# Optimization experiments

Hardware: AMD Instinct MI355X
Metric: run time of the kernel (lower is better)

The kernel has to match this reference:

```python
import jax, jax.numpy as jnp
import numpy as np

B, IN, HID, OUT = 16384, 1024, 4096, 1024
E, K, SIG = 8, 2, 32
ROUTER_IN = IN + SIG + 3  # 1059


def setup_inputs() -> dict:
    key = jax.random.key(0)
    ks = jax.random.split(key, 10)
    sc = lambda k, shape, fan_in: (jax.random.normal(k, shape, jnp.float32)
                                   * (1.0 / np.sqrt(fan_in)))
    return {
        "x": jax.random.normal(ks[0], (B, IN), jnp.float32),
        "physical_signature": jax.random.normal(ks[1], (B, SIG), jnp.float32),
        "task_context": jax.random.uniform(ks[2], (B, 1), jnp.float32),
        "resource_state": jax.random.uniform(ks[3], (B, 2), jnp.float32),
        "router_w1": sc(ks[4], (ROUTER_IN, 2 * E), ROUTER_IN),
        "router_b1": jnp.zeros((2 * E,), jnp.float32),
        "router_w2": sc(ks[5], (2 * E, E), 2 * E),
        "router_b2": jnp.zeros((E,), jnp.float32),
        "expert_w1": sc(ks[6], (E, IN, HID), IN),
        "expert_b1": jnp.zeros((E, HID), jnp.float32),
        "expert_w2": sc(ks[7], (E, HID, OUT), HID),
        "expert_b2": jnp.zeros((E, OUT), jnp.float32),
    }


def reference(x, physical_signature, task_context, resource_state,
              router_w1, router_b1, router_w2, router_b2,
              expert_w1, expert_b1, expert_w2, expert_b2):
    # Router: Linear -> GELU(exact) -> Linear over [x; sig; tc; rs]
    combined = jnp.concatenate(
        [x, physical_signature, task_context, resource_state], axis=-1)
    h = jax.nn.gelu(combined @ router_w1 + router_b1, approximate=False)
    logits = h @ router_w2 + router_b2                      # [B, E]
    weights = jax.nn.softmax(logits, axis=-1)
    top_w, top_idx = jax.lax.top_k(weights, K)              # [B, K]
    # Per-token per-expert combine weight (0 if expert not in top-k)
    c = jnp.einsum("bk,bke->be", top_w,
                   jax.nn.one_hot(top_idx, E, dtype=top_w.dtype))  # [B, E]
    # Dispatch/combine: weighted sum of MLP expert outputs (loop over
    # fixed small E; tokens not routed to expert j have c[:, j] == 0)
    out = jnp.zeros((x.shape[0], OUT), x.dtype)
    for j in range(E):
        hj = jax.nn.gelu(x @ expert_w1[j] + expert_b1[j], approximate=False)
        yj = hj @ expert_w2[j] + expert_b2[j]               # [B, OUT]
        out = out + c[:, j:j + 1] * yj
    return out
```

## Files before the change

### kernel.cpp

```cpp
#include <hip/hip_runtime.h>
#include <math.h>


#define B_TOK 16384
#define IN_D 1024
#define HID_D 4096
#define OUT_D 1024
#define NEXP 8
#define SIG_D 32
#define RIN 1059

#define TILE 128
#define BK 16
#define ROWS_MAX 33792

#define CTRL_COUNTS 0
#define CTRL_CURS 8
#define CTRL_OFFS 16

typedef float f32x4 __attribute__((ext_vector_type(4)));
typedef _Float16 f16x8 __attribute__((ext_vector_type(8)));
typedef short s16x8 __attribute__((ext_vector_type(8)));

__device__ __forceinline__ float gelu_exact(float v) {
    return 0.5f * v * (1.0f + erff(v * 0.70710678118654752440f));
}

__device__ __forceinline__ unsigned short f2h(float f) {
    _Float16 h = (_Float16)f;
    unsigned short u;
    __builtin_memcpy(&u, &h, 2);
    return u;
}

__device__ __forceinline__ void gl16(const unsigned short* g, unsigned short* lds) {
    __builtin_amdgcn_global_load_lds(
        (const __attribute__((address_space(1))) void*)g,
        (__attribute__((address_space(3))) void*)lds, 16, 0, 0);
}


__global__ void zero_ctrl_kernel(int* ctrl) {
    if (threadIdx.x < 32) ctrl[threadIdx.x] = 0;
}

__global__ void zero_out_kernel(float4* out, int n4) {
    int i = blockIdx.x * blockDim.x + threadIdx.x;
    int stride = gridDim.x * blockDim.x;
    for (; i < n4; i += stride) out[i] = make_float4(0.f, 0.f, 0.f, 0.f);
}

__global__ __launch_bounds__(256)
void router_kernel(const float* __restrict__ x, const float* __restrict__ sig,
                   const float* __restrict__ tc, const float* __restrict__ rs,
                   const float* __restrict__ rw1, const float* __restrict__ rb1,
                   const float* __restrict__ rw2, const float* __restrict__ rb2,
                   int* __restrict__ ctrl, int* __restrict__ tt_idx,
                   float2* __restrict__ tt_w) {
    const int wave = threadIdx.x >> 6;
    const int lane = threadIdx.x & 63;
    const int t = blockIdx.x * 4 + wave;

    float acc[16];
#pragma unroll
    for (int j = 0; j < 16; ++j) acc[j] = 0.f;

    for (int i = lane; i < RIN; i += 64) {
        float xv;
        if (i < IN_D) xv = x[(size_t)t * IN_D + i];
        else if (i < IN_D + SIG_D) xv = sig[(size_t)t * SIG_D + (i - IN_D)];
        else if (i == IN_D + SIG_D) xv = tc[t];
        else xv = rs[(size_t)t * 2 + (i - (IN_D + SIG_D + 1))];
        const float4* wr = (const float4*)(rw1 + (size_t)i * 16);
        float4 wa = wr[0], wb = wr[1], wc = wr[2], wd = wr[3];
        acc[0]  = fmaf(xv, wa.x, acc[0]);  acc[1]  = fmaf(xv, wa.y, acc[1]);
        acc[2]  = fmaf(xv, wa.z, acc[2]);  acc[3]  = fmaf(xv, wa.w, acc[3]);
        acc[4]  = fmaf(xv, wb.x, acc[4]);  acc[5]  = fmaf(xv, wb.y, acc[5]);
        acc[6]  = fmaf(xv, wb.z, acc[6]);  acc[7]  = fmaf(xv, wb.w, acc[7]);
        acc[8]  = fmaf(xv, wc.x, acc[8]);  acc[9]  = fmaf(xv, wc.y, acc[9]);
        acc[10] = fmaf(xv, wc.z, acc[10]); acc[11] = fmaf(xv, wc.w, acc[11]);
        acc[12] = fmaf(xv, wd.x, acc[12]); acc[13] = fmaf(xv, wd.y, acc[13]);
        acc[14] = fmaf(xv, wd.z, acc[14]); acc[15] = fmaf(xv, wd.w, acc[15]);
    }
#pragma unroll
    for (int off = 32; off > 0; off >>= 1) {
#pragma unroll
        for (int j = 0; j < 16; ++j) acc[j] += __shfl_xor(acc[j], off, 64);
    }

    float h[16];
#pragma unroll
    for (int j = 0; j < 16; ++j) h[j] = gelu_exact(acc[j] + rb1[j]);

    float logits[8];
#pragma unroll
    for (int e = 0; e < 8; ++e) {
        float s = rb2[e];
#pragma unroll
        for (int j = 0; j < 16; ++j) s = fmaf(h[j], rw2[j * 8 + e], s);
        logits[e] = s;
    }
    float m = logits[0];
#pragma unroll
    for (int e = 1; e < 8; ++e) m = fmaxf(m, logits[e]);
    float p[8];
    float sum = 0.f;
#pragma unroll
    for (int e = 0; e < 8; ++e) { p[e] = expf(logits[e] - m); sum += p[e]; }
    float inv = 1.f / sum;
#pragma unroll
    for (int e = 0; e < 8; ++e) p[e] *= inv;

    int i1 = 0; float w1v = p[0];
#pragma unroll
    for (int e = 1; e < 8; ++e) if (p[e] > w1v) { w1v = p[e]; i1 = e; }
    int i2 = -1; float w2v = -1.f;
#pragma unroll
    for (int e = 0; e < 8; ++e) if (e != i1 && p[e] > w2v) { w2v = p[e]; i2 = e; }

    if (lane == 0) {
        tt_idx[t] = i1 | (i2 << 8);
        tt_w[t] = make_float2(w1v, w2v);
        atomicAdd(&ctrl[CTRL_COUNTS + i1], 1);
        atomicAdd(&ctrl[CTRL_COUNTS + i2], 1);
    }
}

__global__ void finalize_kernel(int* __restrict__ ctrl, int* __restrict__ row_token,
                                float* __restrict__ row_w) {
    if (threadIdx.x == 0) {
        int off = 0;
        for (int e = 0; e < NEXP; ++e) {
            ctrl[CTRL_OFFS + e] = off;
            ctrl[CTRL_CURS + e] = off;
            int c = ctrl[CTRL_COUNTS + e];
            off += (c + TILE - 1) & ~(TILE - 1);
        }
        ctrl[CTRL_OFFS + NEXP] = off;
    }
    for (int i = threadIdx.x; i < ROWS_MAX; i += blockDim.x) {
        row_token[i] = 0;
        row_w[i] = 0.f;
    }
}

__global__ void scatter_kernel(const int* __restrict__ tt_idx,
                               const float2* __restrict__ tt_w,
                               int* __restrict__ ctrl, int* __restrict__ row_token,
                               float* __restrict__ row_w) {
    int t = blockIdx.x * blockDim.x + threadIdx.x;
    if (t >= B_TOK) return;
    int packed = tt_idx[t];
    float2 w = tt_w[t];
    int e1 = packed & 0xff, e2 = (packed >> 8) & 0xff;
    int p1 = atomicAdd(&ctrl[CTRL_CURS + e1], 1);
    row_token[p1] = t; row_w[p1] = w.x;
    int p2 = atomicAdd(&ctrl[CTRL_CURS + e2], 1);
    row_token[p2] = t; row_w[p2] = w.y;
}


__global__ __launch_bounds__(256)
void conv_x_f16(const float* __restrict__ x, unsigned short* __restrict__ xf) {
    size_t i = ((size_t)blockIdx.x * 256 + threadIdx.x) * 8;
    float4 v0 = *(const float4*)(x + i);
    float4 v1 = *(const float4*)(x + i + 4);
    s16x8 vh;
    vh[0] = (short)f2h(v0.x); vh[1] = (short)f2h(v0.y);
    vh[2] = (short)f2h(v0.z); vh[3] = (short)f2h(v0.w);
    vh[4] = (short)f2h(v1.x); vh[5] = (short)f2h(v1.y);
    vh[6] = (short)f2h(v1.z); vh[7] = (short)f2h(v1.w);
    *(s16x8*)(xf + i) = vh;
}

__global__ __launch_bounds__(256)
void conv_w_f16(const float* __restrict__ w, unsigned short* __restrict__ dst,
                int K, int N) {
    const int e = blockIdx.z, nt = blockIdx.x, kt = blockIdx.y;
    __shared__ float tile[64][65];
    const float* src = w + (size_t)e * K * N;
    const int t = threadIdx.x;
#pragma unroll
    for (int p = 0; p < 4; ++p) {
        int kl = (t >> 4) + p * 16, nl = (t & 15) * 4;
        const float* s = src + (size_t)(kt * 64 + kl) * N + nt * 64 + nl;
        float4 v = *(const float4*)s;
        tile[kl][nl] = v.x; tile[kl][nl + 1] = v.y;
        tile[kl][nl + 2] = v.z; tile[kl][nl + 3] = v.w;
    }
    __syncthreads();
#pragma unroll
    for (int p = 0; p < 4; ++p) {
        int nl = (t >> 4) + p * 16, kl = (t & 15) * 4;
        ushort4 h4;
        h4.x = f2h(tile[kl][nl]);
        h4.y = f2h(tile[kl + 1][nl]);
        h4.z = f2h(tile[kl + 2][nl]);
        h4.w = f2h(tile[kl + 3][nl]);
        size_t off = ((size_t)e * N + nt * 64 + nl) * K + kt * 64 + kl;
        *(ushort4*)(dst + off) = h4;
    }
}


__global__ __launch_bounds__(256)
void mm1_f16(const unsigned short* __restrict__ xf, const unsigned short* __restrict__ wf,
             const float* __restrict__ bia, const int* __restrict__ ctrl,
             const int* __restrict__ row_token, unsigned short* __restrict__ hid,
             int rbase) {
    const int total = ctrl[CTRL_OFFS + NEXP];
    const int bper = (int)gridDim.x >> 3;
    const int lin = ((int)blockIdx.x & 7) * bper + ((int)blockIdx.x >> 3);
    const int ty = lin >> 5, tx = lin & 31;
    const int rtile = rbase + ty * TILE;
    if (rtile >= total) return;
    int e = 0;
#pragma unroll
    for (int j = 1; j < NEXP; ++j) if (rtile >= ctrl[CTRL_OFFS + j]) e = j;
    const int ntile = tx * TILE;

    __shared__ unsigned short As[2 * 128 * 32], Bs[2 * 128 * 32];

    const int tid = threadIdx.x;
    const int l = tid & 63, w = tid >> 6;
    const int l15 = l & 15, l4 = l >> 4;
    const int wr = w >> 1, wc = w & 1;

    const int srow = l >> 2, sslot = l & 3;
    const int ar0 = 32 * w + srow, ar1 = ar0 + 16;
    const int kc0 = sslot ^ ((ar0 >> 1) & 3);
    const int kc1 = sslot ^ ((ar1 >> 1) & 3);

    const int tok0 = row_token[rtile + ar0];
    const int tok1 = row_token[rtile + ar1];
    const unsigned short* a0 = xf + (size_t)tok0 * IN_D + kc0 * 8;
    const unsigned short* a1 = xf + (size_t)tok1 * IN_D + kc1 * 8;
    const unsigned short* wb = wf + ((size_t)e * HID_D + ntile) * (size_t)IN_D;
    const unsigned short* b0 = wb + (size_t)ar0 * IN_D + kc0 * 8;
    const unsigned short* b1p = wb + (size_t)ar1 * IN_D + kc1 * 8;

    const int d0 = (32 * w) * 32, d1 = d0 + 16 * 32;

    int aoff[4], boff[4];
#pragma unroll
    for (int mf = 0; mf < 4; ++mf) {
        int r = wr * 64 + mf * 16 + l15;
        aoff[mf] = r * 32 + ((l4 ^ ((r >> 1) & 3)) * 8);
    }
#pragma unroll
    for (int nf = 0; nf < 4; ++nf) {
        int c = wc * 64 + nf * 16 + l15;
        boff[nf] = c * 32 + ((l4 ^ ((c >> 1) & 3)) * 8);
    }

    f32x4 acc[4][4];
#pragma unroll
    for (int i = 0; i < 4; ++i)
#pragma unroll
        for (int j = 0; j < 4; ++j) acc[i][j] = (f32x4){0.f, 0.f, 0.f, 0.f};

    gl16(a0, &As[d0]); gl16(a1, &As[d1]);
    gl16(b0, &Bs[d0]); gl16(b1p, &Bs[d1]);
    __syncthreads();
    int cur = 0;
    for (int k0 = 0; k0 < IN_D; k0 += 32) {
        const int nxt = k0 + 32;
        if (nxt < IN_D) {
            const int bo = (cur ^ 1) * 4096;
            gl16(a0 + nxt, &As[bo + d0]); gl16(a1 + nxt, &As[bo + d1]);
            gl16(b0 + nxt, &Bs[bo + d0]); gl16(b1p + nxt, &Bs[bo + d1]);
        }
        const int ro = cur * 4096;
        f16x8 af[4], bf_[4];
#pragma unroll
        for (int i = 0; i < 4; ++i) af[i] = *(const f16x8*)&As[ro + aoff[i]];
#pragma unroll
        for (int i = 0; i < 4; ++i) bf_[i] = *(const f16x8*)&Bs[ro + boff[i]];
#pragma unroll
        for (int mf = 0; mf < 4; ++mf)
#pragma unroll
            for (int nf = 0; nf < 4; ++nf)
                acc[mf][nf] = __builtin_amdgcn_mfma_f32_16x16x32_f16(af[mf], bf_[nf], acc[mf][nf], 0, 0, 0);
        __syncthreads();
        cur ^= 1;
    }

    float bval[4];
#pragma unroll
    for (int nf = 0; nf < 4; ++nf)
        bval[nf] = bia[(size_t)e * HID_D + ntile + wc * 64 + nf * 16 + l15];
    const size_t hbase = (size_t)(rtile - rbase);
#pragma unroll
    for (int mf = 0; mf < 4; ++mf)
#pragma unroll
        for (int r = 0; r < 4; ++r) {
            size_t row = hbase + wr * 64 + mf * 16 + l4 * 4 + r;
            size_t ro = row * HID_D + ntile + wc * 64 + l15;
#pragma unroll
            for (int nf = 0; nf < 4; ++nf)
                hid[ro + nf * 16] = f2h(gelu_exact(acc[mf][nf][r] + bval[nf]));
        }
}

__global__ __launch_bounds__(256)
void mm2_f16(const unsigned short* __restrict__ hid, const unsigned short* __restrict__ wf,
             const float* __restrict__ bia, const int* __restrict__ ctrl,
             const int* __restrict__ row_token, const float* __restrict__ row_w,
             float* __restrict__ out, int rbase) {
    const int total = ctrl[CTRL_OFFS + NEXP];
    const int bper = (int)gridDim.x >> 3;
    const int lin = ((int)blockIdx.x & 7) * bper + ((int)blockIdx.x >> 3);
    const int ty = lin >> 3, tx = lin & 7;
    const int rtile = rbase + ty * TILE;
    if (rtile >= total) return;
    int e = 0;
#pragma unroll
    for (int j = 1; j < NEXP; ++j) if (rtile >= ctrl[CTRL_OFFS + j]) e = j;
    const int ntile = tx * TILE;

    __shared__ unsigned short As[2 * 128 * 32], Bs[2 * 128 * 32];

    const int tid = threadIdx.x;
    const int l = tid & 63, w = tid >> 6;
    const int l15 = l & 15, l4 = l >> 4;
    const int wr = w >> 1, wc = w & 1;

    const int srow = l >> 2, sslot = l & 3;
    const int ar0 = 32 * w + srow, ar1 = ar0 + 16;
    const int kc0 = sslot ^ ((ar0 >> 1) & 3);
    const int kc1 = sslot ^ ((ar1 >> 1) & 3);

    const size_t lr0 = (size_t)(rtile - rbase) + ar0;
    const unsigned short* a0 = hid + lr0 * HID_D + kc0 * 8;
    const unsigned short* a1 = hid + (lr0 + 16) * HID_D + kc1 * 8;
    const unsigned short* wb = wf + ((size_t)e * OUT_D + ntile) * (size_t)HID_D;
    const unsigned short* b0 = wb + (size_t)ar0 * HID_D + kc0 * 8;
    const unsigned short* b1p = wb + (size_t)ar1 * HID_D + kc1 * 8;

    const int d0 = (32 * w) * 32, d1 = d0 + 16 * 32;

    int aoff[4], boff[4];
#pragma unroll
    for (int mf = 0; mf < 4; ++mf) {
        int r = wr * 64 + mf * 16 + l15;
        aoff[mf] = r * 32 + ((l4 ^ ((r >> 1) & 3)) * 8);
    }
#pragma unroll
    for (int nf = 0; nf < 4; ++nf) {
        int c = wc * 64 + nf * 16 + l15;
        boff[nf] = c * 32 + ((l4 ^ ((c >> 1) & 3)) * 8);
    }

    f32x4 acc[4][4];
#pragma unroll
    for (int i = 0; i < 4; ++i)
#pragma unroll
        for (int j = 0; j < 4; ++j) acc[i][j] = (f32x4){0.f, 0.f, 0.f, 0.f};

    gl16(a0, &As[d0]); gl16(a1, &As[d1]);
    gl16(b0, &Bs[d0]); gl16(b1p, &Bs[d1]);
    __syncthreads();
    int cur = 0;
    for (int k0 = 0; k0 < HID_D; k0 += 32) {
        const int nxt = k0 + 32;
        if (nxt < HID_D) {
            const int bo = (cur ^ 1) * 4096;
            gl16(a0 + nxt, &As[bo + d0]); gl16(a1 + nxt, &As[bo + d1]);
            gl16(b0 + nxt, &Bs[bo + d0]); gl16(b1p + nxt, &Bs[bo + d1]);
        }
        const int ro = cur * 4096;
        f16x8 af[4], bf_[4];
#pragma unroll
        for (int i = 0; i < 4; ++i) af[i] = *(const f16x8*)&As[ro + aoff[i]];
#pragma unroll
        for (int i = 0; i < 4; ++i) bf_[i] = *(const f16x8*)&Bs[ro + boff[i]];
#pragma unroll
        for (int mf = 0; mf < 4; ++mf)
#pragma unroll
            for (int nf = 0; nf < 4; ++nf)
                acc[mf][nf] = __builtin_amdgcn_mfma_f32_16x16x32_f16(af[mf], bf_[nf], acc[mf][nf], 0, 0, 0);
        __syncthreads();
        cur ^= 1;
    }

    float bval[4];
#pragma unroll
    for (int nf = 0; nf < 4; ++nf)
        bval[nf] = bia[(size_t)e * OUT_D + ntile + wc * 64 + nf * 16 + l15];
#pragma unroll
    for (int mf = 0; mf < 4; ++mf)
#pragma unroll
        for (int r = 0; r < 4; ++r) {
            int rg = rtile + wr * 64 + mf * 16 + l4 * 4 + r;
            float wv = row_w[rg];
            if (wv != 0.f) {
                int tok = row_token[rg];
                float* op = out + (size_t)tok * OUT_D + ntile + wc * 64 + l15;
#pragma unroll
                for (int nf = 0; nf < 4; ++nf)
                    atomicAdd(op + nf * 16, wv * (acc[mf][nf][r] + bval[nf]));
            }
        }
}


__global__ __launch_bounds__(256)
void expert_gemm1(const float* __restrict__ x, const float* __restrict__ w1,
                  const float* __restrict__ b1, const int* __restrict__ ctrl,
                  const int* __restrict__ row_token, float* __restrict__ hidden,
                  int rbase) {
    const int total = ctrl[CTRL_OFFS + NEXP];
    const int rtile = rbase + blockIdx.y * TILE;
    if (rtile >= total) return;
    int e = 0;
#pragma unroll
    for (int j = 1; j < NEXP; ++j) if (rtile >= ctrl[CTRL_OFFS + j]) e = j;

    const float* __restrict__ W = w1 + (size_t)e * IN_D * HID_D;
    const float* __restrict__ bias = b1 + (size_t)e * HID_D;
    const int ntile = blockIdx.x * TILE;

    __shared__ float As[BK][TILE];
    __shared__ float Bs[BK][TILE];

    const int tid = threadIdx.x;
    const int tx = tid & 15, ty = tid >> 4;
    const int tm0 = ty * 8, tn0 = tx * 8;

    const int arow = tid >> 1;
    const int akk = (tid & 1) * 8;
    const int tok = row_token[rtile + arow];
    const float* __restrict__ xrow = x + (size_t)tok * IN_D + akk;

    const int bkk = tid >> 4;
    const int bn = (tid & 15) * 8;
    const float* __restrict__ wrow = W + (size_t)bkk * HID_D + ntile + bn;

    float acc[8][8];
#pragma unroll
    for (int i = 0; i < 8; ++i)
#pragma unroll
        for (int j = 0; j < 8; ++j) acc[i][j] = 0.f;

    for (int k0 = 0; k0 < IN_D; k0 += BK) {
        float4 a0 = *(const float4*)(xrow + k0);
        float4 a1 = *(const float4*)(xrow + k0 + 4);
        float4 bv0 = *(const float4*)(wrow + (size_t)k0 * HID_D);
        float4 bv1 = *(const float4*)(wrow + (size_t)k0 * HID_D + 4);
        __syncthreads();
        As[akk + 0][arow] = a0.x; As[akk + 1][arow] = a0.y;
        As[akk + 2][arow] = a0.z; As[akk + 3][arow] = a0.w;
        As[akk + 4][arow] = a1.x; As[akk + 5][arow] = a1.y;
        As[akk + 6][arow] = a1.z; As[akk + 7][arow] = a1.w;
        *(float4*)&Bs[bkk][bn] = bv0;
        *(float4*)&Bs[bkk][bn + 4] = bv1;
        __syncthreads();
#pragma unroll
        for (int k = 0; k < BK; ++k) {
            float a_[8], b_[8];
            *(float4*)&a_[0] = *(const float4*)&As[k][tm0];
            *(float4*)&a_[4] = *(const float4*)&As[k][tm0 + 4];
            *(float4*)&b_[0] = *(const float4*)&Bs[k][tn0];
            *(float4*)&b_[4] = *(const float4*)&Bs[k][tn0 + 4];
#pragma unroll
            for (int i = 0; i < 8; ++i)
#pragma unroll
                for (int j = 0; j < 8; ++j) acc[i][j] = fmaf(a_[i], b_[j], acc[i][j]);
        }
    }

    float bb[8];
#pragma unroll
    for (int j = 0; j < 8; ++j) bb[j] = bias[ntile + tn0 + j];
#pragma unroll
    for (int i = 0; i < 8; ++i) {
        const int grow = rtile + tm0 + i;
        float* hp = hidden + (size_t)(grow - rbase) * HID_D + ntile + tn0;
        float o[8];
#pragma unroll
        for (int j = 0; j < 8; ++j) o[j] = gelu_exact(acc[i][j] + bb[j]);
        *(float4*)hp = make_float4(o[0], o[1], o[2], o[3]);
        *(float4*)(hp + 4) = make_float4(o[4], o[5], o[6], o[7]);
    }
}

__global__ __launch_bounds__(256)
void expert_gemm2(const float* __restrict__ hidden, const float* __restrict__ w2,
                  const float* __restrict__ b2, const int* __restrict__ ctrl,
                  const int* __restrict__ row_token, const float* __restrict__ row_w,
                  float* __restrict__ out, int rbase) {
    const int total = ctrl[CTRL_OFFS + NEXP];
    const int rtile = rbase + blockIdx.y * TILE;
    if (rtile >= total) return;
    int e = 0;
#pragma unroll
    for (int j = 1; j < NEXP; ++j) if (rtile >= ctrl[CTRL_OFFS + j]) e = j;

    const float* __restrict__ W = w2 + (size_t)e * HID_D * OUT_D;
    const float* __restrict__ bias = b2 + (size_t)e * OUT_D;
    const int ntile = blockIdx.x * TILE;

    __shared__ float As[BK][TILE];
    __shared__ float Bs[BK][TILE];

    const int tid = threadIdx.x;
    const int tx = tid & 15, ty = tid >> 4;
    const int tm0 = ty * 8, tn0 = tx * 8;

    const int arow = tid >> 1;
    const int akk = (tid & 1) * 8;
    const float* __restrict__ hrow =
        hidden + (size_t)(rtile - rbase + arow) * HID_D + akk;

    const int bkk = tid >> 4;
    const int bn = (tid & 15) * 8;
    const float* __restrict__ wrow = W + (size_t)bkk * OUT_D + ntile + bn;

    float acc[8][8];
#pragma unroll
    for (int i = 0; i < 8; ++i)
#pragma unroll
        for (int j = 0; j < 8; ++j) acc[i][j] = 0.f;

    for (int k0 = 0; k0 < HID_D; k0 += BK) {
        float4 a0 = *(const float4*)(hrow + k0);
        float4 a1 = *(const float4*)(hrow + k0 + 4);
        float4 bv0 = *(const float4*)(wrow + (size_t)k0 * OUT_D);
        float4 bv1 = *(const float4*)(wrow + (size_t)k0 * OUT_D + 4);
        __syncthreads();
        As[akk + 0][arow] = a0.x; As[akk + 1][arow] = a0.y;
        As[akk + 2][arow] = a0.z; As[akk + 3][arow] = a0.w;
        As[akk + 4][arow] = a1.x; As[akk + 5][arow] = a1.y;
        As[akk + 6][arow] = a1.z; As[akk + 7][arow] = a1.w;
        *(float4*)&Bs[bkk][bn] = bv0;
        *(float4*)&Bs[bkk][bn + 4] = bv1;
        __syncthreads();
#pragma unroll
        for (int k = 0; k < BK; ++k) {
            float a_[8], b_[8];
            *(float4*)&a_[0] = *(const float4*)&As[k][tm0];
            *(float4*)&a_[4] = *(const float4*)&As[k][tm0 + 4];
            *(float4*)&b_[0] = *(const float4*)&Bs[k][tn0];
            *(float4*)&b_[4] = *(const float4*)&Bs[k][tn0 + 4];
#pragma unroll
            for (int i = 0; i < 8; ++i)
#pragma unroll
                for (int j = 0; j < 8; ++j) acc[i][j] = fmaf(a_[i], b_[j], acc[i][j]);
        }
    }

    float bb[8];
#pragma unroll
    for (int j = 0; j < 8; ++j) bb[j] = bias[ntile + tn0 + j];
#pragma unroll
    for (int i = 0; i < 8; ++i) {
        const int grow = rtile + tm0 + i;
        const float wv = row_w[grow];
        if (wv != 0.f) {
            const int tok = row_token[grow];
            float* op = out + (size_t)tok * OUT_D + ntile + tn0;
#pragma unroll
            for (int j = 0; j < 8; ++j) atomicAdd(op + j, wv * (acc[i][j] + bb[j]));
        }
    }
}


extern "C" void kernel_launch(void* const* d_in, const int* in_sizes, int n_in,
                              void* d_out, int out_size, void* d_ws, size_t ws_size,
                              hipStream_t stream) {
    const float* x   = (const float*)d_in[0];
    const float* sig = (const float*)d_in[1];
    const float* tc  = (const float*)d_in[2];
    const float* rs  = (const float*)d_in[3];
    const float* rw1 = (const float*)d_in[4];
    const float* rb1 = (const float*)d_in[5];
    const float* rw2 = (const float*)d_in[6];
    const float* rb2 = (const float*)d_in[7];
    const float* ew1 = (const float*)d_in[8];
    const float* eb1 = (const float*)d_in[9];
    const float* ew2 = (const float*)d_in[10];
    const float* eb2 = (const float*)d_in[11];
    float* out = (float*)d_out;

    char* ws = (char*)d_ws;
    int* ctrl = (int*)ws;
    int* tt_idx = (int*)(ws + 4096);
    float2* tt_w = (float2*)(ws + 69632);
    int* row_token = (int*)(ws + 200704);
    float* row_w = (float*)(ws + 335872);
    const size_t MAPS_END = 471040;

    const size_t XB = (size_t)B_TOK * IN_D * 2;
    const size_t W1B = (size_t)NEXP * IN_D * HID_D * 2;
    const size_t W2B = (size_t)NEXP * HID_D * OUT_D * 2;
    unsigned short* xf  = (unsigned short*)(ws + MAPS_END);
    unsigned short* w1f = (unsigned short*)(ws + MAPS_END + XB);
    unsigned short* w2f = (unsigned short*)(ws + MAPS_END + XB + W1B);
    const size_t FIX16 = MAPS_END + XB + W1B + W2B;

    const bool maps_ok = ws_size >= MAPS_END;
    const bool fp32_ok = ws_size >= MAPS_END + (size_t)TILE * HID_D * 4;
    const bool f16_ok  = ws_size >= FIX16 + (size_t)TILE * HID_D * 2;

    hipLaunchKernelGGL(zero_out_kernel, dim3(2048), dim3(256), 0, stream,
                       (float4*)out, B_TOK * OUT_D / 4);
    if (!maps_ok) return;

    hipLaunchKernelGGL(zero_ctrl_kernel, dim3(1), dim3(64), 0, stream, ctrl);
    hipLaunchKernelGGL(router_kernel, dim3(B_TOK / 4), dim3(256), 0, stream,
                       x, sig, tc, rs, rw1, rb1, rw2, rb2, ctrl, tt_idx, tt_w);
    hipLaunchKernelGGL(finalize_kernel, dim3(1), dim3(256), 0, stream,
                       ctrl, row_token, row_w);
    hipLaunchKernelGGL(scatter_kernel, dim3(B_TOK / 256), dim3(256), 0, stream,
                       tt_idx, tt_w, ctrl, row_token, row_w);

    if (f16_ok) {
        size_t avail = ws_size - FIX16;
        long long q = (long long)(avail / ((size_t)HID_D * 2));
        int qrows = (int)(q > ROWS_MAX ? ROWS_MAX : q);
        qrows &= ~(TILE - 1);
        unsigned short* hid = (unsigned short*)(ws + FIX16);
        const int ngroups = (ROWS_MAX + qrows - 1) / qrows;

        hipLaunchKernelGGL(conv_x_f16, dim3(B_TOK * IN_D / 8 / 256), dim3(256),
                           0, stream, x, xf);
        hipLaunchKernelGGL(conv_w_f16, dim3(HID_D / 64, IN_D / 64, NEXP), dim3(256),
                           0, stream, ew1, w1f, IN_D, HID_D);
        hipLaunchKernelGGL(conv_w_f16, dim3(OUT_D / 64, HID_D / 64, NEXP), dim3(256),
                           0, stream, ew2, w2f, HID_D, OUT_D);

        const int ny = qrows / TILE;
        for (int g = 0; g < ngroups; ++g) {
            const int rbase = g * qrows;
            hipLaunchKernelGGL(mm1_f16, dim3(32 * ny), dim3(256), 0, stream,
                               xf, w1f, eb1, ctrl, row_token, hid, rbase);
            hipLaunchKernelGGL(mm2_f16, dim3(8 * ny), dim3(256), 0, stream,
                               hid, w2f, eb2, ctrl, row_token, row_w, out, rbase);
        }
    } else if (fp32_ok) {
        float* hidden = (float*)(ws + MAPS_END);
        size_t avail = ws_size - MAPS_END;
        long long q = (long long)(avail / ((size_t)HID_D * sizeof(float)));
        int qrows = (int)(q > ROWS_MAX ? ROWS_MAX : q);
        qrows &= ~(TILE - 1);
        const int ngroups = (ROWS_MAX + qrows - 1) / qrows;
        for (int g = 0; g < ngroups; ++g) {
            const int rbase = g * qrows;
            hipLaunchKernelGGL(expert_gemm1, dim3(HID_D / TILE, qrows / TILE), dim3(256),
                               0, stream, x, ew1, eb1, ctrl, row_token, hidden, rbase);
            hipLaunchKernelGGL(expert_gemm2, dim3(OUT_D / TILE, qrows / TILE), dim3(256),
                               0, stream, hidden, ew2, eb2, ctrl, row_token, row_w, out, rbase);
        }
    }
}
```

Baseline: 1.858 ms.

## Triple-buffer LDS tiles with two-stage-ahead prefetch in expert GEMMs

Replaces the double-buffered K loop in both expert GEMM kernels with a three-stage LDS ring, prefetching two K-steps ahead. Each phase waits with a partial vmcnt and a raw s_barrier instead of a full __syncthreads, so global loads stay in flight across iterations. The loop is manually unrolled by three with fixed buffer indices. The cost is 50% more shared memory per block, which may lower occupancy, and hand-written waitcnt logic that relies on the exact count of outstanding loads.

```diff
diff --git a/kernel.cpp b/kernel.cpp
--- a/kernel.cpp
+++ b/kernel.cpp
@@ -203,6 +203,55 @@
 }
 
 
+#define MMPHASE(P, KS, VM)                                                   \
+    {                                                                        \
+        gl16(a0 + (KS), &As[((P) + 2) % 3 * 4096 + d0]);                     \
+        gl16(a1 + (KS), &As[((P) + 2) % 3 * 4096 + d1]);                     \
+        gl16(b0 + (KS), &Bs[((P) + 2) % 3 * 4096 + d0]);                     \
+        gl16(b1p + (KS), &Bs[((P) + 2) % 3 * 4096 + d1]);                    \
+        f16x8 af[4], bf_[4];                                                 \
+        _Pragma("unroll") for (int i = 0; i < 4; ++i)                        \
+            af[i] = *(const f16x8*)&As[(P) * 4096 + aoff[i]];                \
+        _Pragma("unroll") for (int i = 0; i < 4; ++i)                        \
+            bf_[i] = *(const f16x8*)&Bs[(P) * 4096 + boff[i]];               \
+        _Pragma("unroll") for (int mf = 0; mf < 4; ++mf)                     \
+            _Pragma("unroll") for (int nf = 0; nf < 4; ++nf)                 \
+                acc[mf][nf] = __builtin_amdgcn_mfma_f32_16x16x32_f16(        \
+                    af[mf], bf_[nf], acc[mf][nf], 0, 0, 0);                  \
+        asm volatile("s_waitcnt vmcnt(" #VM ")" ::: "memory");               \
+        __builtin_amdgcn_s_barrier();                                        \
+        __builtin_amdgcn_sched_barrier(0);                                   \
+    }
+
+#define MMPHASE_NOSTAGE(P, VM)                                               \
+    {                                                                        \
+        f16x8 af[4], bf_[4];                                                 \
+        _Pragma("unroll") for (int i = 0; i < 4; ++i)                        \
+            af[i] = *(const f16x8*)&As[(P) * 4096 + aoff[i]];                \
+        _Pragma("unroll") for (int i = 0; i < 4; ++i)                        \
+            bf_[i] = *(const f16x8*)&Bs[(P) * 4096 + boff[i]];               \
+        _Pragma("unroll") for (int mf = 0; mf < 4; ++mf)                     \
+            _Pragma("unroll") for (int nf = 0; nf < 4; ++nf)                 \
+                acc[mf][nf] = __builtin_amdgcn_mfma_f32_16x16x32_f16(        \
+                    af[mf], bf_[nf], acc[mf][nf], 0, 0, 0);                  \
+        asm volatile("s_waitcnt vmcnt(" #VM ")" ::: "memory");               \
+        __builtin_amdgcn_s_barrier();                                        \
+        __builtin_amdgcn_sched_barrier(0);                                   \
+    }
+
+#define MMPHASE_FINAL(P)                                                     \
+    {                                                                        \
+        f16x8 af[4], bf_[4];                                                 \
+        _Pragma("unroll") for (int i = 0; i < 4; ++i)                        \
+            af[i] = *(const f16x8*)&As[(P) * 4096 + aoff[i]];                \
+        _Pragma("unroll") for (int i = 0; i < 4; ++i)                        \
+            bf_[i] = *(const f16x8*)&Bs[(P) * 4096 + boff[i]];               \
+        _Pragma("unroll") for (int mf = 0; mf < 4; ++mf)                     \
+            _Pragma("unroll") for (int nf = 0; nf < 4; ++nf)                 \
+                acc[mf][nf] = __builtin_amdgcn_mfma_f32_16x16x32_f16(        \
+                    af[mf], bf_[nf], acc[mf][nf], 0, 0, 0);                  \
+    }
+
 __global__ __launch_bounds__(256)
 void mm1_f16(const unsigned short* __restrict__ xf, const unsigned short* __restrict__ wf,
              const float* __restrict__ bia, const int* __restrict__ ctrl,
@@ -219,7 +268,7 @@
     for (int j = 1; j < NEXP; ++j) if (rtile >= ctrl[CTRL_OFFS + j]) e = j;
     const int ntile = tx * TILE;
 
-    __shared__ unsigned short As[2 * 128 * 32], Bs[2 * 128 * 32];
+    __shared__ unsigned short As[3 * 128 * 32], Bs[3 * 128 * 32];
 
     const int tid = threadIdx.x;
     const int l = tid & 63, w = tid >> 6;
@@ -261,29 +310,21 @@
 
     gl16(a0, &As[d0]); gl16(a1, &As[d1]);
     gl16(b0, &Bs[d0]); gl16(b1p, &Bs[d1]);
-    __syncthreads();
-    int cur = 0;
-    for (int k0 = 0; k0 < IN_D; k0 += 32) {
-        const int nxt = k0 + 32;
-        if (nxt < IN_D) {
-            const int bo = (cur ^ 1) * 4096;
-            gl16(a0 + nxt, &As[bo + d0]); gl16(a1 + nxt, &As[bo + d1]);
-            gl16(b0 + nxt, &Bs[bo + d0]); gl16(b1p + nxt, &Bs[bo + d1]);
-        }
-        const int ro = cur * 4096;
-        f16x8 af[4], bf_[4];
-#pragma unroll
-        for (int i = 0; i < 4; ++i) af[i] = *(const f16x8*)&As[ro + aoff[i]];
-#pragma unroll
-        for (int i = 0; i < 4; ++i) bf_[i] = *(const f16x8*)&Bs[ro + boff[i]];
-#pragma unroll
-        for (int mf = 0; mf < 4; ++mf)
-#pragma unroll
-            for (int nf = 0; nf < 4; ++nf)
-                acc[mf][nf] = __builtin_amdgcn_mfma_f32_16x16x32_f16(af[mf], bf_[nf], acc[mf][nf], 0, 0, 0);
-        __syncthreads();
-        cur ^= 1;
-    }
+    gl16(a0 + 32, &As[4096 + d0]); gl16(a1 + 32, &As[4096 + d1]);
+    gl16(b0 + 32, &Bs[4096 + d0]); gl16(b1p + 32, &Bs[4096 + d1]);
+    asm volatile("s_waitcnt vmcnt(4)" ::: "memory");
+    __builtin_amdgcn_s_barrier();
+    __builtin_amdgcn_sched_barrier(0);
+
+    int ks = 64;
+    for (int t = 0; t < 30; t += 3) {
+        MMPHASE(0, ks, 4);
+        MMPHASE(1, ks + 32, 4);
+        MMPHASE(2, ks + 64, 4);
+        ks += 96;
+    }
+    MMPHASE_NOSTAGE(0, 0);
+    MMPHASE_FINAL(1);
 
     float bval[4];
 #pragma unroll
@@ -318,7 +359,7 @@
     for (int j = 1; j < NEXP; ++j) if (rtile >= ctrl[CTRL_OFFS + j]) e = j;
     const int ntile = tx * TILE;
 
-    __shared__ unsigned short As[2 * 128 * 32], Bs[2 * 128 * 32];
+    __shared__ unsigned short As[3 * 128 * 32], Bs[3 * 128 * 32];
 
     const int tid = threadIdx.x;
     const int l = tid & 63, w = tid >> 6;
@@ -359,29 +400,21 @@
 
     gl16(a0, &As[d0]); gl16(a1, &As[d1]);
     gl16(b0, &Bs[d0]); gl16(b1p, &Bs[d1]);
-    __syncthreads();
-    int cur = 0;
-    for (int k0 = 0; k0 < HID_D; k0 += 32) {
-        const int nxt = k0 + 32;
-        if (nxt < HID_D) {
-            const int bo = (cur ^ 1) * 4096;
-            gl16(a0 + nxt, &As[bo + d0]); gl16(a1 + nxt, &As[bo + d1]);
-            gl16(b0 + nxt, &Bs[bo + d0]); gl16(b1p + nxt, &Bs[bo + d1]);
-        }
-        const int ro = cur * 4096;
-        f16x8 af[4], bf_[4];
-#pragma unroll
-        for (int i = 0; i < 4; ++i) af[i] = *(const f16x8*)&As[ro + aoff[i]];
-#pragma unroll
-        for (int i = 0; i < 4; ++i) bf_[i] = *(const f16x8*)&Bs[ro + boff[i]];
-#pragma unroll
-        for (int mf = 0; mf < 4; ++mf)
-#pragma unroll
-            for (int nf = 0; nf < 4; ++nf)
-                acc[mf][nf] = __builtin_amdgcn_mfma_f32_16x16x32_f16(af[mf], bf_[nf], acc[mf][nf], 0, 0, 0);
-        __syncthreads();
-        cur ^= 1;
-    }
+    gl16(a0 + 32, &As[4096 + d0]); gl16(a1 + 32, &As[4096 + d1]);
+    gl16(b0 + 32, &Bs[4096 + d0]); gl16(b1p + 32, &Bs[4096 + d1]);
+    asm volatile("s_waitcnt vmcnt(4)" ::: "memory");
+    __builtin_amdgcn_s_barrier();
+    __builtin_amdgcn_sched_barrier(0);
+
+    int ks = 64;
+    for (int t = 0; t < 126; t += 3) {
+        MMPHASE(0, ks, 4);
+        MMPHASE(1, ks + 32, 4);
+        MMPHASE(2, ks + 64, 4);
+        ks += 96;
+    }
+    MMPHASE_NOSTAGE(0, 0);
+    MMPHASE_FINAL(1);
 
     float bval[4];
 #pragma unroll
```

Result: slower. 2.321 ms (+24.9%).

## Use 256x256 tiles with 512 threads and triple-buffered LDS pipeline in expert GEMMs

Applied to the files above, without the earlier changes.

Grows the output tile of both expert GEMMs from 128x128 to 256x256, using 8 waves per block and 32 accumulators per wave, and pads expert segments to 256 rows. The K loop becomes a triple-buffered pipeline with explicit waitcnt, split barriers and MFMA priority raising, so global loads overlap compute. Block-to-XCD remapping now also handles grids not divisible by 8. Larger tiles give more reuse per byte loaded but add padding waste, register pressure and fewer blocks.

```diff
diff --git a/kernel.cpp b/kernel.cpp
--- a/kernel.cpp
+++ b/kernel.cpp
@@ -12,7 +12,8 @@
 
 #define TILE 128
 #define BK 16
-#define ROWS_MAX 33792
+#define EPAD 256
+#define ROWS_MAX 34816
 
 #define CTRL_COUNTS 0
 #define CTRL_CURS 8
@@ -134,7 +135,7 @@
             ctrl[CTRL_OFFS + e] = off;
             ctrl[CTRL_CURS + e] = off;
             int c = ctrl[CTRL_COUNTS + e];
-            off += (c + TILE - 1) & ~(TILE - 1);
+            off += (c + EPAD - 1) & ~(EPAD - 1);
         }
         ctrl[CTRL_OFFS + NEXP] = off;
     }
@@ -203,87 +204,144 @@
 }
 
 
-__global__ __launch_bounds__(256)
+#define MMT_CORE0(P)                                                          \
+    {                                                                         \
+        _Pragma("unroll") for (int i = 0; i < 4; ++i)                         \
+            af[i] = *(const f16x8*)&As[(P) * 8192 + aoff[i]];                 \
+        _Pragma("unroll") for (int i = 0; i < 4; ++i)                         \
+            bf[i] = *(const f16x8*)&Bs[(P) * 8192 + boff[i]];                 \
+    }
+#define MMT_CORE1(P)                                                          \
+    {                                                                         \
+        _Pragma("unroll") for (int i = 0; i < 4; ++i)                         \
+            af[i] = *(const f16x8*)&As[(P) * 8192 + aoff[4 + i]];             \
+    }
+#define MMT_MFMA(MB)                                                          \
+    __builtin_amdgcn_s_setprio(1);                                            \
+    _Pragma("unroll") for (int mf = 0; mf < 4; ++mf)                          \
+        _Pragma("unroll") for (int nf = 0; nf < 4; ++nf)                      \
+            acc[(MB) + mf][nf] = __builtin_amdgcn_mfma_f32_16x16x32_f16(      \
+                af[mf], bf[nf], acc[(MB) + mf][nf], 0, 0, 0);                 \
+    __builtin_amdgcn_s_setprio(0);
+
+#define MMTILE(P, KS, VM)                                                     \
+    {                                                                         \
+        f16x8 af[4], bf[4];                                                   \
+        MMT_CORE0(P)                                                          \
+        gl16(ga0 + (KS), &As[((P) + 2) % 3 * 8192 + ad0]);                    \
+        gl16(ga1 + (KS), &As[((P) + 2) % 3 * 8192 + ad1]);                    \
+        __builtin_amdgcn_s_barrier();                                         \
+        asm volatile("s_waitcnt lgkmcnt(0)" ::: "memory");                    \
+        MMT_MFMA(0)                                                           \
+        __builtin_amdgcn_s_barrier();                                         \
+        MMT_CORE1(P)                                                          \
+        gl16(gb0 + (KS), &Bs[((P) + 2) % 3 * 8192 + ad0]);                    \
+        gl16(gb1 + (KS), &Bs[((P) + 2) % 3 * 8192 + ad1]);                    \
+        __builtin_amdgcn_s_barrier();                                         \
+        asm volatile("s_waitcnt lgkmcnt(0)" ::: "memory");                    \
+        MMT_MFMA(4)                                                           \
+        asm volatile("s_waitcnt vmcnt(" #VM ")" ::: "memory");                \
+        __builtin_amdgcn_s_barrier();                                         \
+    }
+
+#define MMTILE_NOSTAGE(P)                                                     \
+    {                                                                         \
+        f16x8 af[4], bf[4];                                                   \
+        MMT_CORE0(P)                                                          \
+        __builtin_amdgcn_s_barrier();                                         \
+        asm volatile("s_waitcnt lgkmcnt(0)" ::: "memory");                    \
+        MMT_MFMA(0)                                                           \
+        __builtin_amdgcn_s_barrier();                                         \
+        MMT_CORE1(P)                                                          \
+        asm volatile("s_waitcnt lgkmcnt(0)" ::: "memory");                    \
+        MMT_MFMA(4)                                                           \
+        asm volatile("s_waitcnt vmcnt(0)" ::: "memory");                      \
+        __builtin_amdgcn_s_barrier();                                         \
+    }
+
+#define MMTILE_FINAL(P)                                                       \
+    {                                                                         \
+        f16x8 af[4], bf[4];                                                   \
+        MMT_CORE0(P)                                                          \
+        asm volatile("s_waitcnt lgkmcnt(0)" ::: "memory");                    \
+        MMT_MFMA(0)                                                           \
+        MMT_CORE1(P)                                                          \
+        asm volatile("s_waitcnt lgkmcnt(0)" ::: "memory");                    \
+        MMT_MFMA(4)                                                           \
+    }
+
+
+__global__ __launch_bounds__(512)
 void mm1_f16(const unsigned short* __restrict__ xf, const unsigned short* __restrict__ wf,
              const float* __restrict__ bia, const int* __restrict__ ctrl,
              const int* __restrict__ row_token, unsigned short* __restrict__ hid,
              int rbase) {
     const int total = ctrl[CTRL_OFFS + NEXP];
-    const int bper = (int)gridDim.x >> 3;
-    const int lin = ((int)blockIdx.x & 7) * bper + ((int)blockIdx.x >> 3);
-    const int ty = lin >> 5, tx = lin & 31;
-    const int rtile = rbase + ty * TILE;
+    const int nwg = (int)gridDim.x, bid = (int)blockIdx.x;
+    const int q = nwg >> 3, r8 = nwg & 7, xcd = bid & 7;
+    const int lin = (xcd < r8 ? xcd * (q + 1) : r8 * (q + 1) + (xcd - r8) * q) + (bid >> 3);
+    const int ty = lin >> 4, tx = lin & 15;
+    const int rtile = rbase + ty * 256;
     if (rtile >= total) return;
     int e = 0;
 #pragma unroll
     for (int j = 1; j < NEXP; ++j) if (rtile >= ctrl[CTRL_OFFS + j]) e = j;
-    const int ntile = tx * TILE;
-
-    __shared__ unsigned short As[2 * 128 * 32], Bs[2 * 128 * 32];
+    const int ntile = tx * 256;
+
+    __shared__ unsigned short As[3 * 8192], Bs[3 * 8192];
 
     const int tid = threadIdx.x;
     const int l = tid & 63, w = tid >> 6;
     const int l15 = l & 15, l4 = l >> 4;
-    const int wr = w >> 1, wc = w & 1;
-
-    const int srow = l >> 2, sslot = l & 3;
-    const int ar0 = 32 * w + srow, ar1 = ar0 + 16;
-    const int kc0 = sslot ^ ((ar0 >> 1) & 3);
-    const int kc1 = sslot ^ ((ar1 >> 1) & 3);
-
-    const int tok0 = row_token[rtile + ar0];
-    const int tok1 = row_token[rtile + ar1];
-    const unsigned short* a0 = xf + (size_t)tok0 * IN_D + kc0 * 8;
-    const unsigned short* a1 = xf + (size_t)tok1 * IN_D + kc1 * 8;
+    const int wr = w >> 2, wc = w & 3;
+
+    const int c0 = tid, c1 = 512 + tid;
+    const int arow0 = c0 >> 2, arow1 = c1 >> 2;
+    const int kc0 = (c0 & 3) ^ ((arow0 >> 1) & 3);
+    const int kc1 = (c1 & 3) ^ ((arow1 >> 1) & 3);
+    const int tok0 = row_token[rtile + arow0];
+    const int tok1 = row_token[rtile + arow1];
+    const unsigned short* ga0 = xf + (size_t)tok0 * IN_D + kc0 * 8;
+    const unsigned short* ga1 = xf + (size_t)tok1 * IN_D + kc1 * 8;
     const unsigned short* wb = wf + ((size_t)e * HID_D + ntile) * (size_t)IN_D;
-    const unsigned short* b0 = wb + (size_t)ar0 * IN_D + kc0 * 8;
-    const unsigned short* b1p = wb + (size_t)ar1 * IN_D + kc1 * 8;
-
-    const int d0 = (32 * w) * 32, d1 = d0 + 16 * 32;
-
-    int aoff[4], boff[4];
-#pragma unroll
-    for (int mf = 0; mf < 4; ++mf) {
-        int r = wr * 64 + mf * 16 + l15;
-        aoff[mf] = r * 32 + ((l4 ^ ((r >> 1) & 3)) * 8);
+    const unsigned short* gb0 = wb + (size_t)arow0 * IN_D + kc0 * 8;
+    const unsigned short* gb1 = wb + (size_t)arow1 * IN_D + kc1 * 8;
+    const int ad0 = w * 512, ad1 = 4096 + w * 512;
+
+    int aoff[8], boff[4];
+#pragma unroll
+    for (int mf = 0; mf < 8; ++mf) {
+        int rr = wr * 128 + mf * 16 + l15;
+        aoff[mf] = rr * 32 + ((l4 ^ ((rr >> 1) & 3)) * 8);
     }
 #pragma unroll
     for (int nf = 0; nf < 4; ++nf) {
-        int c = wc * 64 + nf * 16 + l15;
-        boff[nf] = c * 32 + ((l4 ^ ((c >> 1) & 3)) * 8);
-    }
-
-    f32x4 acc[4][4];
-#pragma unroll
-    for (int i = 0; i < 4; ++i)
+        int nn = wc * 64 + nf * 16 + l15;
+        boff[nf] = nn * 32 + ((l4 ^ ((nn >> 1) & 3)) * 8);
+    }
+
+    f32x4 acc[8][4];
+#pragma unroll
+    for (int i = 0; i < 8; ++i)
 #pragma unroll
         for (int j = 0; j < 4; ++j) acc[i][j] = (f32x4){0.f, 0.f, 0.f, 0.f};
 
-    gl16(a0, &As[d0]); gl16(a1, &As[d1]);
-    gl16(b0, &Bs[d0]); gl16(b1p, &Bs[d1]);
-    __syncthreads();
-    int cur = 0;
-    for (int k0 = 0; k0 < IN_D; k0 += 32) {
-        const int nxt = k0 + 32;
-        if (nxt < IN_D) {
-            const int bo = (cur ^ 1) * 4096;
-            gl16(a0 + nxt, &As[bo + d0]); gl16(a1 + nxt, &As[bo + d1]);
-            gl16(b0 + nxt, &Bs[bo + d0]); gl16(b1p + nxt, &Bs[bo + d1]);
-        }
-        const int ro = cur * 4096;
-        f16x8 af[4], bf_[4];
-#pragma unroll
-        for (int i = 0; i < 4; ++i) af[i] = *(const f16x8*)&As[ro + aoff[i]];
-#pragma unroll
-        for (int i = 0; i < 4; ++i) bf_[i] = *(const f16x8*)&Bs[ro + boff[i]];
-#pragma unroll
-        for (int mf = 0; mf < 4; ++mf)
-#pragma unroll
-            for (int nf = 0; nf < 4; ++nf)
-                acc[mf][nf] = __builtin_amdgcn_mfma_f32_16x16x32_f16(af[mf], bf_[nf], acc[mf][nf], 0, 0, 0);
-        __syncthreads();
-        cur ^= 1;
-    }
+    gl16(ga0, &As[ad0]); gl16(ga1, &As[ad1]);
+    gl16(gb0, &Bs[ad0]); gl16(gb1, &Bs[ad1]);
+    gl16(ga0 + 32, &As[8192 + ad0]); gl16(ga1 + 32, &As[8192 + ad1]);
+    gl16(gb0 + 32, &Bs[8192 + ad0]); gl16(gb1 + 32, &Bs[8192 + ad1]);
+    asm volatile("s_waitcnt vmcnt(4)" ::: "memory");
+    __builtin_amdgcn_s_barrier();
+
+    int ks = 64;
+    for (int t = 0; t < 30; t += 3) {
+        MMTILE(0, ks, 4);
+        MMTILE(1, ks + 32, 4);
+        MMTILE(2, ks + 64, 4);
+        ks += 96;
+    }
+    MMTILE_NOSTAGE(0);
+    MMTILE_FINAL(1);
 
     float bval[4];
 #pragma unroll
@@ -291,114 +349,104 @@
         bval[nf] = bia[(size_t)e * HID_D + ntile + wc * 64 + nf * 16 + l15];
     const size_t hbase = (size_t)(rtile - rbase);
 #pragma unroll
-    for (int mf = 0; mf < 4; ++mf)
-#pragma unroll
-        for (int r = 0; r < 4; ++r) {
-            size_t row = hbase + wr * 64 + mf * 16 + l4 * 4 + r;
+    for (int mf = 0; mf < 8; ++mf)
+#pragma unroll
+        for (int rr = 0; rr < 4; ++rr) {
+            size_t row = hbase + wr * 128 + mf * 16 + l4 * 4 + rr;
             size_t ro = row * HID_D + ntile + wc * 64 + l15;
 #pragma unroll
             for (int nf = 0; nf < 4; ++nf)
-                hid[ro + nf * 16] = f2h(gelu_exact(acc[mf][nf][r] + bval[nf]));
+                hid[ro + nf * 16] = f2h(gelu_exact(acc[mf][nf][rr] + bval[nf]));
         }
 }
 
-__global__ __launch_bounds__(256)
+__global__ __launch_bounds__(512)
 void mm2_f16(const unsigned short* __restrict__ hid, const unsigned short* __restrict__ wf,
              const float* __restrict__ bia, const int* __restrict__ ctrl,
              const int* __restrict__ row_token, const float* __restrict__ row_w,
              float* __restrict__ out, int rbase) {
     const int total = ctrl[CTRL_OFFS + NEXP];
-    const int bper = (int)gridDim.x >> 3;
-    const int lin = ((int)blockIdx.x & 7) * bper + ((int)blockIdx.x >> 3);
-    const int ty = lin >> 3, tx = lin & 7;
-    const int rtile = rbase + ty * TILE;
+    const int nwg = (int)gridDim.x, bid = (int)blockIdx.x;
+    const int q = nwg >> 3, r8 = nwg & 7, xcd = bid & 7;
+    const int lin = (xcd < r8 ? xcd * (q + 1) : r8 * (q + 1) + (xcd - r8) * q) + (bid >> 3);
+    const int ty = lin >> 2, tx = lin & 3;
+    const int rtile = rbase + ty * 256;
     if (rtile >= total) return;
     int e = 0;
 #pragma unroll
     for (int j = 1; j < NEXP; ++j) if (rtile >= ctrl[CTRL_OFFS + j]) e = j;
-    const int ntile = tx * TILE;
-
-    __shared__ unsigned short As[2 * 128 * 32], Bs[2 * 128 * 32];
+    const int ntile = tx * 256;
+
+    __shared__ unsigned short As[3 * 8192], Bs[3 * 8192];
 
     const int tid = threadIdx.x;
     const int l = tid & 63, w = tid >> 6;
     const int l15 = l & 15, l4 = l >> 4;
-    const int wr = w >> 1, wc = w & 1;
-
-    const int srow = l >> 2, sslot = l & 3;
-    const int ar0 = 32 * w + srow, ar1 = ar0 + 16;
-    const int kc0 = sslot ^ ((ar0 >> 1) & 3);
-    const int kc1 = sslot ^ ((ar1 >> 1) & 3);
-
-    const size_t lr0 = (size_t)(rtile - rbase) + ar0;
-    const unsigned short* a0 = hid + lr0 * HID_D + kc0 * 8;
-    const unsigned short* a1 = hid + (lr0 + 16) * HID_D + kc1 * 8;
+    const int wr = w >> 2, wc = w & 3;
+
+    const int c0 = tid, c1 = 512 + tid;
+    const int arow0 = c0 >> 2, arow1 = c1 >> 2;
+    const int kc0 = (c0 & 3) ^ ((arow0 >> 1) & 3);
+    const int kc1 = (c1 & 3) ^ ((arow1 >> 1) & 3);
+    const size_t lr0 = (size_t)(rtile - rbase);
+    const unsigned short* ga0 = hid + (lr0 + arow0) * HID_D + kc0 * 8;
+    const unsigned short* ga1 = hid + (lr0 + arow1) * HID_D + kc1 * 8;
     const unsigned short* wb = wf + ((size_t)e * OUT_D + ntile) * (size_t)HID_D;
-    const unsigned short* b0 = wb + (size_t)ar0 * HID_D + kc0 * 8;
-    const unsigned short* b1p = wb + (size_t)ar1 * HID_D + kc1 * 8;
-
-    const int d0 = (32 * w) * 32, d1 = d0 + 16 * 32;
-
-    int aoff[4], boff[4];
-#pragma unroll
-    for (int mf = 0; mf < 4; ++mf) {
-        int r = wr * 64 + mf * 16 + l15;
-        aoff[mf] = r * 32 + ((l4 ^ ((r >> 1) & 3)) * 8);
+    const unsigned short* gb0 = wb + (size_t)arow0 * HID_D + kc0 * 8;
+    const unsigned short* gb1 = wb + (size_t)arow1 * HID_D + kc1 * 8;
+    const int ad0 = w * 512, ad1 = 4096 + w * 512;
+
+    int aoff[8], boff[4];
+#pragma unroll
+    for (int mf = 0; mf < 8; ++mf) {
+        int rr = wr * 128 + mf * 16 + l15;
+        aoff[mf] = rr * 32 + ((l4 ^ ((rr >> 1) & 3)) * 8);
     }
 #pragma unroll
     for (int nf = 0; nf < 4; ++nf) {
-        int c = wc * 64 + nf * 16 + l15;
-        boff[nf] = c * 32 + ((l4 ^ ((c >> 1) & 3)) * 8);
-    }
-
-    f32x4 acc[4][4];
-#pragma unroll
-    for (int i = 0; i < 4; ++i)
+        int nn = wc * 64 + nf * 16 + l15;
+        boff[nf] = nn * 32 + ((l4 ^ ((nn >> 1) & 3)) * 8);
+    }
+
+    f32x4 acc[8][4];
+#pragma unroll
+    for (int i = 0; i < 8; ++i)
 #pragma unroll
         for (int j = 0; j < 4; ++j) acc[i][j] = (f32x4){0.f, 0.f, 0.f, 0.f};
 
-    gl16(a0, &As[d0]); gl16(a1, &As[d1]);
-    gl16(b0, &Bs[d0]); gl16(b1p, &Bs[d1]);
-    __syncthreads();
-    int cur = 0;
-    for (int k0 = 0; k0 < HID_D; k0 += 32) {
-        const int nxt = k0 + 32;
-        if (nxt < HID_D) {
-            const int bo = (cur ^ 1) * 4096;
-            gl16(a0 + nxt, &As[bo + d0]); gl16(a1 + nxt, &As[bo + d1]);
-            gl16(b0 + nxt, &Bs[bo + d0]); gl16(b1p + nxt, &Bs[bo + d1]);
-        }
-        const int ro = cur * 4096;
-        f16x8 af[4], bf_[4];
-#pragma unroll
-        for (int i = 0; i < 4; ++i) af[i] = *(const f16x8*)&As[ro + aoff[i]];
-#pragma unroll
-        for (int i = 0; i < 4; ++i) bf_[i] = *(const f16x8*)&Bs[ro + boff[i]];
-#pragma unroll
-        for (int mf = 0; mf < 4; ++mf)
-#pragma unroll
-            for (int nf = 0; nf < 4; ++nf)
-                acc[mf][nf] = __builtin_amdgcn_mfma_f32_16x16x32_f16(af[mf], bf_[nf], acc[mf][nf], 0, 0, 0);
-        __syncthreads();
-        cur ^= 1;
-    }
+    gl16(ga0, &As[ad0]); gl16(ga1, &As[ad1]);
+    gl16(gb0, &Bs[ad0]); gl16(gb1, &Bs[ad1]);
+    gl16(ga0 + 32, &As[8192 + ad0]); gl16(ga1 + 32, &As[8192 + ad1]);
+    gl16(gb0 + 32, &Bs[8192 + ad0]); gl16(gb1 + 32, &Bs[8192 + ad1]);
+    asm volatile("s_waitcnt vmcnt(4)" ::: "memory");
+    __builtin_amdgcn_s_barrier();
+
+    int ks = 64;
+    for (int t = 0; t < 126; t += 3) {
+        MMTILE(0, ks, 4);
+        MMTILE(1, ks + 32, 4);
+        MMTILE(2, ks + 64, 4);
+        ks += 96;
+    }
+    MMTILE_NOSTAGE(0);
+    MMTILE_FINAL(1);
 
     float bval[4];
 #pragma unroll
     for (int nf = 0; nf < 4; ++nf)
         bval[nf] = bia[(size_t)e * OUT_D + ntile + wc * 64 + nf * 16 + l15];
 #pragma unroll
-    for (int mf = 0; mf < 4; ++mf)
-#pragma unroll
-        for (int r = 0; r < 4; ++r) {
-            int rg = rtile + wr * 64 + mf * 16 + l4 * 4 + r;
+    for (int mf = 0; mf < 8; ++mf)
+#pragma unroll
+        for (int rr = 0; rr < 4; ++rr) {
+            int rg = rtile + wr * 128 + mf * 16 + l4 * 4 + rr;
             float wv = row_w[rg];
             if (wv != 0.f) {
                 int tok = row_token[rg];
                 float* op = out + (size_t)tok * OUT_D + ntile + wc * 64 + l15;
 #pragma unroll
                 for (int nf = 0; nf < 4; ++nf)
-                    atomicAdd(op + nf * 16, wv * (acc[mf][nf][r] + bval[nf]));
+                    atomicAdd(op + nf * 16, wv * (acc[mf][nf][rr] + bval[nf]));
             }
         }
 }
@@ -588,8 +636,8 @@
     int* tt_idx = (int*)(ws + 4096);
     float2* tt_w = (float2*)(ws + 69632);
     int* row_token = (int*)(ws + 200704);
-    float* row_w = (float*)(ws + 335872);
-    const size_t MAPS_END = 471040;
+    float* row_w = (float*)(ws + 339968);
+    const size_t MAPS_END = 479232;
 
     const size_t XB = (size_t)B_TOK * IN_D * 2;
     const size_t W1B = (size_t)NEXP * IN_D * HID_D * 2;
@@ -601,7 +649,7 @@
 
     const bool maps_ok = ws_size >= MAPS_END;
     const bool fp32_ok = ws_size >= MAPS_END + (size_t)TILE * HID_D * 4;
-    const bool f16_ok  = ws_size >= FIX16 + (size_t)TILE * HID_D * 2;
+    const bool f16_ok  = ws_size >= FIX16 + (size_t)256 * HID_D * 2;
 
     hipLaunchKernelGGL(zero_out_kernel, dim3(2048), dim3(256), 0, stream,
                        (float4*)out, B_TOK * OUT_D / 4);
@@ -619,7 +667,7 @@
         size_t avail = ws_size - FIX16;
         long long q = (long long)(avail / ((size_t)HID_D * 2));
         int qrows = (int)(q > ROWS_MAX ? ROWS_MAX : q);
-        qrows &= ~(TILE - 1);
+        qrows &= ~255;
         unsigned short* hid = (unsigned short*)(ws + FIX16);
         const int ngroups = (ROWS_MAX + qrows - 1) / qrows;
 
@@ -630,12 +678,12 @@
         hipLaunchKernelGGL(conv_w_f16, dim3(OUT_D / 64, HID_D / 64, NEXP), dim3(256),
                            0, stream, ew2, w2f, HID_D, OUT_D);
 
-        const int ny = qrows / TILE;
+        const int ny = qrows / 256;
         for (int g = 0; g < ngroups; ++g) {
             const int rbase = g * qrows;
-            hipLaunchKernelGGL(mm1_f16, dim3(32 * ny), dim3(256), 0, stream,
+            hipLaunchKernelGGL(mm1_f16, dim3(16 * ny), dim3(512), 0, stream,
                                xf, w1f, eb1, ctrl, row_token, hid, rbase);
-            hipLaunchKernelGGL(mm2_f16, dim3(8 * ny), dim3(256), 0, stream,
+            hipLaunchKernelGGL(mm2_f16, dim3(4 * ny), dim3(512), 0, stream,
                                hid, w2f, eb2, ctrl, row_token, row_w, out, rbase);
         }
     } else if (fp32_ok) {
```

Result: no change. 1.894 ms (+2.0%).
